# Kernel tuning notes

Measured on AMD Instinct MI355X. Metric: run time of the kernel, lower is better.

## Reference

```python
import jax, jax.numpy as jnp
import numpy as np

S, B, C = 7, 2, 20
L_COORD, L_NOOBJ = 5.0, 0.5
IMG, GRID = 448.0, 64.0
EPS = 1e-08


def setup_inputs() -> dict:
    key = jax.random.key(0)
    k = jax.random.split(key, 8)
    N = 16384
    bb = jax.random.uniform(k[0], (N, S, S, 5 * B + C), dtype=jnp.float32)
    # ground truth layout: [0:4] rel coords, [4] unused, [5:9] abs pixel corners, [9] obj flag, [10:30] class
    rel = jax.random.uniform(k[1], (N, S, S, 4), dtype=jnp.float32)
    pad = jax.random.uniform(k[2], (N, S, S, 1), dtype=jnp.float32)
    cx = jax.random.uniform(k[3], (N, S, S), dtype=jnp.float32) * IMG
    cy = jax.random.uniform(k[4], (N, S, S), dtype=jnp.float32) * IMG
    wh = 32.0 + jax.random.uniform(k[5], (N, S, S, 2), dtype=jnp.float32) * 128.0
    x1 = jnp.clip(cx - wh[..., 0] / 2, 0.0, IMG - 1)
    y1 = jnp.clip(cy - wh[..., 1] / 2, 0.0, IMG - 1)
    x2 = jnp.clip(cx + wh[..., 0] / 2, 0.0, IMG - 1)
    y2 = jnp.clip(cy + wh[..., 1] / 2, 0.0, IMG - 1)
    corners = jnp.stack([x1, y1, x2, y2], axis=-1)
    objflag = jax.random.uniform(k[6], (N, S, S, 1), dtype=jnp.float32)  # round -> 0/1
    cls = jax.random.uniform(k[7], (N, S, S, C), dtype=jnp.float32)
    gt = jnp.concatenate([rel, pad, corners, objflag, cls], axis=-1)
    return {"bounding_boxes": bb, "ground_truth": gt}


def _iou(box, gt):
    # box: [N,S,S,5] predicted (rel coords); gt corners gt[...,5:9] in pixels
    cols = jnp.arange(S, dtype=box.dtype)
    gx = (cols * GRID)[None, None, :]  # indexCol * 64
    gy = (cols * GRID)[None, :, None]  # indexRow * 64
    px = jnp.trunc(gx + box[..., 0] * GRID)   # int() cast in original
    py = jnp.trunc(gy + box[..., 1] * GRID)
    pw = jnp.trunc(box[..., 2] * IMG)
    ph = jnp.trunc(box[..., 3] * IMG)
    x1 = jnp.maximum(0.0, px - pw / 2)
    y1 = jnp.maximum(0.0, py - ph / 2)
    x2 = jnp.minimum(IMG - 1, px + pw / 2)
    y2 = jnp.minimum(IMG - 1, py + ph / 2)
    p_area = (x2 - x1) * (y2 - y1)
    g = gt[..., 5:9]
    g_area = (g[..., 2] - g[..., 0]) * (g[..., 3] - g[..., 1])
    lx = jnp.maximum(x1, g[..., 0])
    rx = jnp.minimum(x2, g[..., 2])
    uy = jnp.maximum(y1, g[..., 1])
    dy = jnp.minimum(y2, g[..., 3])
    inter = (rx - lx) * (dy - uy)
    valid = (rx >= lx) & (dy >= uy)
    denom = p_area + g_area - inter
    denom = jnp.where(denom == 0, 1.0, denom)
    return jnp.where(valid, inter / denom, 0.0)


def reference(bounding_boxes, ground_truth):
    bb, gt = bounding_boxes, ground_truth
    b1 = bb[..., 0:5]
    b2 = bb[..., 5:10]
    # in the original, iou goes through .item()/int() so it is a constant wrt autograd
    iou1 = jax.lax.stop_gradient(_iou(b1, gt))
    iou2 = jax.lax.stop_gradient(_iou(b2, gt))
    obj = jnp.round(gt[..., 9]) != 0  # [N,S,S]

    pick1 = iou1 > iou2
    pb = jnp.where(pick1[..., None], b1, b2)     # responsible box
    npb = jnp.where(pick1[..., None], b2, b1)    # other box
    iou_sel = jnp.where(pick1, iou1, iou2)

    coord = L_COORD * (
        (gt[..., 0] - pb[..., 0]) ** 2
        + (gt[..., 1] - pb[..., 1]) ** 2
        + (jnp.sqrt(gt[..., 2] + EPS) - jnp.sqrt(pb[..., 2] + EPS)) ** 2
        + (jnp.sqrt(gt[..., 3] + EPS) - jnp.sqrt(pb[..., 3] + EPS)) ** 2
    )
    conf_obj = (pb[..., 4] - iou_sel) ** 2
    cls = jnp.mean((gt[..., 10:] - bb[..., B * 5:]) ** 2, axis=-1)  # mseLoss (mean)
    noobj_of_obj = L_NOOBJ * npb[..., 4] ** 2
    obj_cell_loss = coord + conf_obj + cls + noobj_of_obj

    noobj_cell_loss = L_NOOBJ * b1[..., 4] ** 2 + b2[..., 4] ** 2

    loss = jnp.sum(jnp.where(obj, obj_cell_loss, noobj_cell_loss))
    loss_coord = jnp.sum(jnp.where(obj, coord, 0.0))
    # note: original python-float accumulator omits l_noobj on the no-predict conf term
    loss_confidence = jnp.sum(jnp.where(obj, conf_obj + npb[..., 4] ** 2, noobj_cell_loss))
    loss_classes = jnp.sum(jnp.where(obj, cls, 0.0))
    iou_sum = jnp.sum(jnp.where(obj, iou_sel, 0.0))
    object_num = jnp.sum(obj.astype(jnp.int32))
    return (loss, loss_coord, loss_confidence, loss_classes, iou_sum, object_num)
```

## Files before the change

kernel.cpp:

```cpp
#include <hip/hip_runtime.h>

#define TPB    64
#define CELLS  64
#define FPC    30
#define TILE_F (CELLS * FPC)

typedef const __attribute__((address_space(1))) void* gptr_t;
typedef __attribute__((address_space(3))) void* lptr_t;


__launch_bounds__(TPB)
__global__ void yolo_loss_kernel(const float* __restrict__ bb,
                                 const float* __restrict__ gt,
                                 float* __restrict__ ws,
                                 int nblocks) {
    __shared__ float sBB[TILE_F];
    __shared__ float sGT[TILE_F];

    const int tid = threadIdx.x;
    const int bid = blockIdx.x;

    const float* __restrict__ bsrc = bb + (size_t)bid * TILE_F;
    const float* __restrict__ gsrc = gt + (size_t)bid * TILE_F;

#pragma unroll
    for (int c = 0; c < 8; ++c) {
        const int of = (c < 7) ? c * 256 : 1664;
        __builtin_amdgcn_global_load_lds((gptr_t)(bsrc + of + tid * 4),
                                         (lptr_t)(&sBB[of]), 16, 0, 0);
        __builtin_amdgcn_global_load_lds((gptr_t)(gsrc + of + tid * 4),
                                         (lptr_t)(&sGT[of]), 16, 0, 0);
    }
    __syncthreads();

    const float* __restrict__ Bp = &sBB[tid * FPC];
    const float* __restrict__ Gp = &sGT[tid * FPC];

    const int cell = bid * CELLS + tid;
    const int w = cell % 49;
    const float gx = (float)(w % 7) * 64.0f;
    const float gy = (float)(w / 7) * 64.0f;

    const float g0 = Gp[5], g1 = Gp[6], g2 = Gp[7], g3 = Gp[8];
    const float g_area = (g2 - g0) * (g3 - g1);

    const float b1x = Bp[0], b1y = Bp[1], b1w = Bp[2], b1h = Bp[3], b1c = Bp[4];
    const float b2x = Bp[5], b2y = Bp[6], b2w = Bp[7], b2h = Bp[8], b2c = Bp[9];

    auto iou_of = [&](float bx, float by, float bw, float bh) -> float {
        float px = truncf(gx + bx * 64.0f);
        float py = truncf(gy + by * 64.0f);
        float pw = truncf(bw * 448.0f);
        float ph = truncf(bh * 448.0f);
        float x1 = fmaxf(0.0f,   px - pw * 0.5f);
        float y1 = fmaxf(0.0f,   py - ph * 0.5f);
        float x2 = fminf(447.0f, px + pw * 0.5f);
        float y2 = fminf(447.0f, py + ph * 0.5f);
        float parea = (x2 - x1) * (y2 - y1);
        float lx = fmaxf(x1, g0), rx = fminf(x2, g2);
        float uy = fmaxf(y1, g1), dn = fminf(y2, g3);
        float inter = (rx - lx) * (dn - uy);
        float denom = parea + g_area - inter;
        denom = (denom == 0.0f) ? 1.0f : denom;
        return ((rx >= lx) && (dn >= uy)) ? (inter / denom) : 0.0f;
    };

    const float iou1 = iou_of(b1x, b1y, b1w, b1h);
    const float iou2 = iou_of(b2x, b2y, b2w, b2h);
    const bool  p1   = iou1 > iou2;

    const float pbx = p1 ? b1x : b2x, pby = p1 ? b1y : b2y;
    const float pbw = p1 ? b1w : b2w, pbh = p1 ? b1h : b2h;
    const float pbc = p1 ? b1c : b2c;
    const float npc = p1 ? b2c : b1c;
    const float iousel = p1 ? iou1 : iou2;

    const bool obj = (rintf(Gp[9]) != 0.0f);

    const float dx = Gp[0] - pbx;
    const float dy = Gp[1] - pby;
    const float dw = sqrtf(Gp[2] + 1e-8f) - sqrtf(pbw + 1e-8f);
    const float dh = sqrtf(Gp[3] + 1e-8f) - sqrtf(pbh + 1e-8f);
    const float coord = 5.0f * (dx * dx + dy * dy + dw * dw + dh * dh);

    float confobj = pbc - iousel;
    confobj *= confobj;

    float cls = 0.f;
#pragma unroll
    for (int k = 0; k < 20; ++k) {
        float d = Gp[10 + k] - Bp[10 + k];
        cls += d * d;
    }
    cls *= (1.0f / 20.0f);

    const float noobj_of_obj = 0.5f * npc * npc;
    const float objloss   = coord + confobj + cls + noobj_of_obj;
    const float noobjloss = 0.5f * b1c * b1c + b2c * b2c;

    float L, Lc, Lconf, Lcls, Isum, On;
    if (obj) {
        L = objloss; Lc = coord; Lconf = confobj + npc * npc;
        Lcls = cls;  Isum = iousel; On = 1.0f;
    } else {
        L = noobjloss; Lc = 0.f; Lconf = noobjloss; Lcls = 0.f; Isum = 0.f; On = 0.f;
    }

    float v[6] = {L, Lc, Lconf, Lcls, Isum, On};
#pragma unroll
    for (int k = 0; k < 6; ++k) {
#pragma unroll
        for (int off = 32; off > 0; off >>= 1)
            v[k] += __shfl_down(v[k], off, 64);
    }
    if (tid == 0) {
#pragma unroll
        for (int k = 0; k < 6; ++k)
            ws[(size_t)k * nblocks + bid] = v[k];
    }
}

__global__ void reduce_partials(const float* __restrict__ ws,
                                float* __restrict__ out, int nblocks) {
    __shared__ float sw[16];
    const int k   = blockIdx.x;
    const int tid = threadIdx.x;
    const float4* __restrict__ w4 = (const float4*)(ws + (size_t)k * nblocks);
    const int nf4 = nblocks >> 2;

    float s = 0.f;
    for (int i = tid; i < nf4; i += blockDim.x) {
        float4 q = w4[i];
        s += (q.x + q.y) + (q.z + q.w);
    }
#pragma unroll
    for (int off = 32; off > 0; off >>= 1)
        s += __shfl_down(s, off, 64);
    if ((tid & 63) == 0) sw[tid >> 6] = s;
    __syncthreads();
    if (tid == 0) {
        float t = 0.f;
#pragma unroll
        for (int j = 0; j < 16; ++j) t += sw[j];
        out[k] = t;
    }
}

extern "C" void kernel_launch(void* const* d_in, const int* in_sizes, int n_in,
                              void* d_out, int out_size, void* d_ws, size_t ws_size,
                              hipStream_t stream) {
    const float* bb = (const float*)d_in[0];
    const float* gt = (const float*)d_in[1];
    float* out = (float*)d_out;
    float* ws  = (float*)d_ws;

    const int ncells = in_sizes[0] / FPC;
    const int grid   = ncells / CELLS;

    yolo_loss_kernel<<<grid, TPB, 0, stream>>>(bb, gt, ws, grid);
    reduce_partials<<<6, 1024, 0, stream>>>(ws, out, grid);
}
```

Baseline: 36.03 us.

## Process four tiles per block with double-buffered async LDS staging

Each block now handles four 64-cell tiles rather than one. The next tile's global-to-LDS loads are issued before the current tile is computed, double-buffered and gated by vmcnt waits, and results accumulate in registers before a single wave reduction. This cuts the block count fourfold, so the final partial reduction has less to sum, and it overlaps memory latency with compute. In exchange each block uses twice the LDS and there are fewer blocks to hide latency through occupancy. The hand-written vmcnt counts must match the number of loads issued per stage.

```diff
diff --git a/kernel.cpp b/kernel.cpp
--- a/kernel.cpp
+++ b/kernel.cpp
@@ -1,42 +1,30 @@
 #include <hip/hip_runtime.h>
 
 #define TPB    64
-#define CELLS  64
 #define FPC    30
-#define TILE_F (CELLS * FPC)
+#define TILE_C 64
+#define TILE_F (TILE_C * FPC)
+#define TILES  4
 
 typedef const __attribute__((address_space(1))) void* gptr_t;
 typedef __attribute__((address_space(3))) void* lptr_t;
 
-
-__launch_bounds__(TPB)
-__global__ void yolo_loss_kernel(const float* __restrict__ bb,
-                                 const float* __restrict__ gt,
-                                 float* __restrict__ ws,
-                                 int nblocks) {
-    __shared__ float sBB[TILE_F];
-    __shared__ float sGT[TILE_F];
-
-    const int tid = threadIdx.x;
-    const int bid = blockIdx.x;
-
-    const float* __restrict__ bsrc = bb + (size_t)bid * TILE_F;
-    const float* __restrict__ gsrc = gt + (size_t)bid * TILE_F;
-
+__device__ __forceinline__ void stage_tile(const float* __restrict__ bsrc,
+                                           const float* __restrict__ gsrc,
+                                           float* dB, float* dG, int lane) {
 #pragma unroll
     for (int c = 0; c < 8; ++c) {
         const int of = (c < 7) ? c * 256 : 1664;
-        __builtin_amdgcn_global_load_lds((gptr_t)(bsrc + of + tid * 4),
-                                         (lptr_t)(&sBB[of]), 16, 0, 0);
-        __builtin_amdgcn_global_load_lds((gptr_t)(gsrc + of + tid * 4),
-                                         (lptr_t)(&sGT[of]), 16, 0, 0);
+        __builtin_amdgcn_global_load_lds((gptr_t)(bsrc + of + lane * 4),
+                                         (lptr_t)(dB + of), 16, 0, 0);
+        __builtin_amdgcn_global_load_lds((gptr_t)(gsrc + of + lane * 4),
+                                         (lptr_t)(dG + of), 16, 0, 0);
     }
-    __syncthreads();
+}
 
-    const float* __restrict__ Bp = &sBB[tid * FPC];
-    const float* __restrict__ Gp = &sGT[tid * FPC];
-
-    const int cell = bid * CELLS + tid;
+__device__ __forceinline__ void do_cell(const float* __restrict__ Bp,
+                                        const float* __restrict__ Gp,
+                                        int cell, float* acc) {
     const int w = cell % 49;
     const float gx = (float)(w % 7) * 64.0f;
     const float gy = (float)(w / 7) * 64.0f;
@@ -98,25 +86,61 @@
     const float objloss   = coord + confobj + cls + noobj_of_obj;
     const float noobjloss = 0.5f * b1c * b1c + b2c * b2c;
 
-    float L, Lc, Lconf, Lcls, Isum, On;
     if (obj) {
-        L = objloss; Lc = coord; Lconf = confobj + npc * npc;
-        Lcls = cls;  Isum = iousel; On = 1.0f;
+        acc[0] += objloss; acc[1] += coord; acc[2] += confobj + npc * npc;
+        acc[3] += cls;     acc[4] += iousel; acc[5] += 1.0f;
     } else {
-        L = noobjloss; Lc = 0.f; Lconf = noobjloss; Lcls = 0.f; Isum = 0.f; On = 0.f;
+        acc[0] += noobjloss; acc[2] += noobjloss;
     }
+}
 
-    float v[6] = {L, Lc, Lconf, Lcls, Isum, On};
+__launch_bounds__(TPB)
+__global__ void yolo_loss_kernel(const float* __restrict__ bb,
+                                 const float* __restrict__ gt,
+                                 float* __restrict__ ws,
+                                 int nblocks) {
+    __shared__ float sBB[2][TILE_F];
+    __shared__ float sGT[2][TILE_F];
+
+    const int lane = threadIdx.x;
+    const int bid  = blockIdx.x;
+
+    const size_t baseF   = (size_t)bid * TILES * TILE_F;
+    const int    cell0   = bid * TILES * TILE_C + lane;
+    const float* __restrict__ bbase = bb + baseF;
+    const float* __restrict__ gbase = gt + baseF;
+
+    float acc[6] = {0.f, 0.f, 0.f, 0.f, 0.f, 0.f};
+
+    stage_tile(bbase, gbase, sBB[0], sGT[0], lane);
+
+#define STEP(T, WAITN_STR)                                                     \
+    do {                                                                       \
+        if ((T) + 1 < TILES)                                                   \
+            stage_tile(bbase + ((T) + 1) * TILE_F, gbase + ((T) + 1) * TILE_F, \
+                       sBB[((T) + 1) & 1], sGT[((T) + 1) & 1], lane);          \
+        asm volatile("s_waitcnt vmcnt(" WAITN_STR ")" ::: "memory");           \
+        __builtin_amdgcn_sched_barrier(0);                                     \
+        do_cell(&sBB[(T) & 1][lane * FPC], &sGT[(T) & 1][lane * FPC],          \
+                cell0 + (T) * TILE_C, acc);                                    \
+    } while (0)
+
+    STEP(0, "16");
+    STEP(1, "16");
+    STEP(2, "16");
+    STEP(3, "0");
+#undef STEP
+
 #pragma unroll
     for (int k = 0; k < 6; ++k) {
 #pragma unroll
         for (int off = 32; off > 0; off >>= 1)
-            v[k] += __shfl_down(v[k], off, 64);
+            acc[k] += __shfl_down(acc[k], off, 64);
     }
-    if (tid == 0) {
+    if (lane == 0) {
 #pragma unroll
         for (int k = 0; k < 6; ++k)
-            ws[(size_t)k * nblocks + bid] = v[k];
+            ws[(size_t)k * nblocks + bid] = acc[k];
     }
 }
 
@@ -155,7 +179,7 @@
     float* ws  = (float*)d_ws;
 
     const int ncells = in_sizes[0] / FPC;
-    const int grid   = ncells / CELLS;
+    const int grid   = ncells / (TILES * TILE_C);
 
     yolo_loss_kernel<<<grid, TPB, 0, stream>>>(bb, gt, ws, grid);
     reduce_partials<<<6, 1024, 0, stream>>>(ws, out, grid);
```

Measured after the change: 37.40 us. 3.8% more time.
